# Optimization experiments

Hardware: AMD Instinct MI355X
Metric: run time of the kernel (lower is better)

## Reference

```python
import jax, jax.numpy as jnp
import numpy as np

# Axial permutations for num_dimensions=3, emb_dim=-1 (total rank 5), att_dims=[1,2,3]
PERMS = [[0, 2, 3, 1, 4], [0, 1, 3, 2, 4], [0, 1, 2, 3, 4]]
H_SELF = 8
H_CROSS = 8
E_HEAD = 64  # dims_embed[0] / (num_heads_self + num_heads_cross) = 1024/16


def layernorm(x, eps=1e-5):
    # nn.LayerNorm(elementwise_affine=False)
    m = x.mean(axis=-1, keepdims=True)
    v = x.var(axis=-1, keepdims=True)
    return (x - m) * jax.lax.rsqrt(v + eps)


def cross_attention(x, kv, wq, wkv, h, e):
    # x: [bb, t, d_q], kv: [bb, t_kv, d_kv]
    q = x @ wq                                   # [bb, t, h*e]
    k, v = jnp.split(kv @ wkv, 2, axis=-1)       # each [bb, t_kv, h*e]
    bb, t = q.shape[0], q.shape[1]
    tk = k.shape[1]
    q = q.reshape(bb, t, h, e)
    k = k.reshape(bb, tk, h, e)
    v = v.reshape(bb, tk, h, e)
    dots = jnp.einsum('bihe,bjhe->bhij', q, k) * (e ** -0.5)
    attn = jax.nn.softmax(dots, axis=-1)
    out = jnp.einsum('bhij,bjhe->bihe', attn, v)
    return out.reshape(bb, t, h * e)


def permute_to_from(x, kv, perm, wq, wkv, h, e):
    inv = list(np.argsort(perm))
    ax = jnp.transpose(x, perm)
    axkv = jnp.transpose(kv, perm)
    shape = list(ax.shape)
    shape_kv = list(axkv.shape)
    t, d = shape[-2], shape[-1]
    t_kv, d_kv = shape_kv[-2], shape_kv[-1]
    r1 = shape[1] / shape_kv[1]
    r2 = shape[2] / shape_kv[2]
    if int(r1) != 1:
        axkv = jnp.repeat(axkv, max(1, int(r1)), axis=1)
        ax = jnp.repeat(ax, max(1, int(1.0 / r1)), axis=1)
    if int(r2) != 1:
        axkv = jnp.repeat(axkv, max(1, int(r2)), axis=2)
        ax = jnp.repeat(ax, max(1, int(1.0 / r2)), axis=2)
    assert ax.shape[1:3] == axkv.shape[1:3]
    perm_shape = list(ax.shape)
    out = cross_attention(ax.reshape(-1, t, d), axkv.reshape(-1, t_kv, d_kv), wq, wkv, h, e)
    out = out.reshape(perm_shape[:-1] + [-1])
    if shape[1] < shape_kv[1]:  # field0 coarser along perm dim 1 -> mean-pool back
        out = out.reshape(shape[:2] + [int(1.0 / r1)] + perm_shape[2:-1] + [-1]).mean(axis=2)
    if shape[2] < shape_kv[2]:
        out = out.reshape(shape[:3] + [int(1.0 / r2)] + perm_shape[3:-1] + [-1]).mean(axis=3)
    out = out.reshape(shape[:-1] + [-1])
    return jnp.transpose(out, inv)


def setup_inputs() -> dict:
    key = jax.random.key(0)
    ks = jax.random.split(key, 8)
    B, T, LA, LO, D0, D1 = 32, 12, 12, 12, 1024, 512
    s = 0.02
    return {
        'x0': jax.random.normal(ks[0], (B, T, LA, LO, D0), dtype=jnp.float32),
        'x1': jax.random.normal(ks[1], (B, T, LA // 2, LO // 2, D1), dtype=jnp.float32),
        'wq_self': jax.random.normal(ks[2], (3, D0, 512), dtype=jnp.float32) * s,
        'wkv_self': jax.random.normal(ks[3], (3, D0, 1024), dtype=jnp.float32) * s,
        'wq_cross': jax.random.normal(ks[4], (3, D0, 512), dtype=jnp.float32) * s,
        'wkv_cross': jax.random.normal(ks[5], (3, D1, 1024), dtype=jnp.float32) * s,
        'w_out': jax.random.normal(ks[6], (3, 1024, D0), dtype=jnp.float32) * s,
        'b_out': jnp.zeros((3, D0), dtype=jnp.float32),
    }


def reference(x0, x1, wq_self, wkv_self, wq_cross, wkv_cross, w_out, b_out):
    pass_through = x0
    f0 = layernorm(x0)
    f1 = layernorm(x1)
    for ip, perm in enumerate(PERMS):
        o_self = permute_to_from(f0, f0, perm, wq_self[ip], wkv_self[ip], H_SELF, E_HEAD)
        o_cross = permute_to_from(f0, f1, perm, wq_cross[ip], wkv_cross[ip], H_CROSS, E_HEAD)
        f0 = jnp.concatenate([o_self, o_cross], axis=-1) @ w_out[ip] + b_out[ip]
    return pass_through + f0
```

## Files before the change

### kernel.cpp

```cpp
#include <hip/hip_runtime.h>
#include <hip/hip_bf16.h>


typedef __bf16 bf16x8 __attribute__((ext_vector_type(8)));
typedef float floatx4 __attribute__((ext_vector_type(4)));
typedef float floatx16 __attribute__((ext_vector_type(16)));

#define N0 55296
#define N1 13824

#define RAW_BARRIER() asm volatile("s_barrier" ::: "memory")
#define VMCNT(n) asm volatile("s_waitcnt vmcnt(" #n ")" ::: "memory")

__device__ __forceinline__ void gload16(const void* g, void* l) {
    __builtin_amdgcn_global_load_lds(
        (const __attribute__((address_space(1))) unsigned int*)g,
        (__attribute__((address_space(3))) unsigned int*)l, 16, 0, 0);
}

template <int SIG>
__device__ __forceinline__ int mapRow(int i) {
    if (SIG == 0) return i;
    const int b = i / 1728, r = i % 1728;
    const int d1 = r / 144, r2 = r % 144, d2 = r2 / 12, d3 = r2 % 12;
    if (SIG == 1) return b * 1728 + d3 * 144 + d1 * 12 + d2;
    if (SIG == 2) return b * 1728 + d3 * 144 + d2 * 12 + d1;
    return b * 1728 + d1 * 144 + d3 * 12 + d2;
}

template <int D>
__device__ __forceinline__ void ln_body(const float* __restrict__ xr,
                                        __hip_bfloat16* __restrict__ yr)
{
    constexpr int V = D / 256;
    const int tid = threadIdx.x;
    float vals[V];
    if constexpr (V == 4) {
        const float4 t4 = *(const float4*)(xr + tid * 4);
        vals[0] = t4.x; vals[1] = t4.y; vals[2] = t4.z; vals[3] = t4.w;
    } else {
        const float2 t2 = *(const float2*)(xr + tid * 2);
        vals[0] = t2.x; vals[1] = t2.y;
    }
    float s = 0.f, q = 0.f;
#pragma unroll
    for (int k = 0; k < V; ++k) { s += vals[k]; q += vals[k] * vals[k]; }
#pragma unroll
    for (int off = 32; off > 0; off >>= 1) {
        s += __shfl_xor(s, off);
        q += __shfl_xor(q, off);
    }
    __shared__ float rs[4], rq[4];
    const int w = tid >> 6;
    if ((tid & 63) == 0) { rs[w] = s; rq[w] = q; }
    __syncthreads();
    s = rs[0] + rs[1] + rs[2] + rs[3];
    q = rq[0] + rq[1] + rq[2] + rq[3];
    const float mean = s * (1.f / D);
    const float var  = q * (1.f / D) - mean * mean;
    const float rstd = rsqrtf(var + 1e-5f);
    __hip_bfloat16 o[V];
#pragma unroll
    for (int k = 0; k < V; ++k) o[k] = __float2bfloat16((vals[k] - mean) * rstd);
    if constexpr (V == 4) *(uint2*)(yr + tid * 4) = *(const uint2*)o;
    else                  *(uint*)(yr + tid * 2)  = *(const uint*)o;
}

__global__ __launch_bounds__(256)
void ln_all(const float* __restrict__ x0, const float* __restrict__ x1,
            __hip_bfloat16* __restrict__ f0, __hip_bfloat16* __restrict__ f1)
{
    const int row = blockIdx.x;
    if (row < N0) {
        ln_body<1024>(x0 + (size_t)row * 1024, f0 + (size_t)row * 1024);
    } else {
        const int r = row - N0;
        ln_body<512>(x1 + (size_t)r * 512, f1 + (size_t)r * 512);
    }
}

__global__ __launch_bounds__(256)
void transpose_all(const float* __restrict__ wqs, const float* __restrict__ wkvs,
                   const float* __restrict__ wqc, const float* __restrict__ wkvc,
                   const float* __restrict__ wo,
                   __hip_bfloat16* __restrict__ W1t,
                   __hip_bfloat16* __restrict__ W2t,
                   __hip_bfloat16* __restrict__ W3t)
{
    int idx = blockIdx.x;
    const float* src;
    __hip_bfloat16* dst;
    int K, N;
    if (idx < 1536) {
        const int ip = idx / 512; idx %= 512; K = 1024; N = 512;
        src = wqs + (size_t)ip * 524288;  dst = W1t + (size_t)ip * 2097152;
    } else if (idx < 4608) {
        idx -= 1536;
        const int ip = idx / 1024; idx %= 1024; K = 1024; N = 1024;
        src = wkvs + (size_t)ip * 1048576; dst = W1t + (size_t)ip * 2097152 + 524288;
    } else if (idx < 6144) {
        idx -= 4608;
        const int ip = idx / 512; idx %= 512; K = 1024; N = 512;
        src = wqc + (size_t)ip * 524288;  dst = W1t + (size_t)ip * 2097152 + 1572864;
    } else if (idx < 7680) {
        idx -= 6144;
        const int ip = idx / 512; idx %= 512; K = 512; N = 1024;
        src = wkvc + (size_t)ip * 524288; dst = W2t + (size_t)ip * 524288;
    } else {
        idx -= 7680;
        const int ip = idx / 1024; idx %= 1024; K = 1024; N = 1024;
        src = wo + (size_t)ip * 1048576;  dst = W3t + (size_t)ip * 1048576;
    }
    const int tiles_x = N >> 5;
    const int n0 = (idx % tiles_x) * 32, k0 = (idx / tiles_x) * 32;

    __shared__ float tile[32][33];
    const int tx = threadIdx.x & 31, ty = threadIdx.x >> 5;
#pragma unroll
    for (int d = 0; d < 4; ++d)
        tile[ty + d * 8][tx] = src[(size_t)(k0 + ty + d * 8) * N + n0 + tx];
    __syncthreads();
#pragma unroll
    for (int d = 0; d < 4; ++d)
        dst[(size_t)(n0 + ty + d * 8) * K + k0 + tx] = __float2bfloat16(tile[tx][ty + d * 8]);
}

__global__ __launch_bounds__(256)
void cast_w3o(const float* __restrict__ wo, __hip_bfloat16* __restrict__ W3o)
{
    const size_t i = ((size_t)blockIdx.x * 256 + threadIdx.x) * 4;
    const float4 v = *(const float4*)(wo + i);
    __hip_bfloat16 o[4] = { __float2bfloat16(v.x), __float2bfloat16(v.y),
                            __float2bfloat16(v.z), __float2bfloat16(v.w) };
    *(uint2*)(W3o + i) = *(const uint2*)o;
}

__global__ __launch_bounds__(256)
void bfold_kernel(const float* __restrict__ b_out,
                  const __hip_bfloat16* __restrict__ W1t,
                  float* __restrict__ bf)
{
    const int idx = blockIdx.x * 256 + threadIdx.x;
    const int j = idx >> 11, n = idx & 2047;
    const float* b = b_out + j * 1024;
    const __hip_bfloat16* w = W1t + ((size_t)(j + 1) * 2048 + n) * 1024;
    float s = 0.f;
#pragma unroll 4
    for (int d = 0; d < 1024; ++d) s += b[d] * __bfloat162float(w[d]);
    bf[idx] = s;
}

template <int EPI, int SIG>
__global__ __launch_bounds__(512)
void gemm8p(const __hip_bfloat16* __restrict__ A,
            const __hip_bfloat16* __restrict__ Bt,
            void* __restrict__ Cv,
            const float* __restrict__ bias,
            const float* __restrict__ resid,
            int M, int N, int K, int lda)
{
    __shared__ __align__(16) char lds[131072];

    const int gx  = gridDim.x;
    const int nwg = gx * gridDim.y;
    const int bid = blockIdx.y * gx + blockIdx.x;
    const int swz = (bid & 7) * (nwg >> 3) + (bid >> 3);
    const int m0 = (swz / gx) * 256;
    const int n0 = (swz % gx) * 256;

    const int t    = threadIdx.x;
    const int w    = t >> 6;
    const int lane = t & 63;
    const int wr   = w >> 2;
    const int wc   = w & 3;
    const int l31  = lane & 31;
    const int kh   = lane >> 5;

    floatx16 acc[4][2] = {};

    const int tr   = t >> 3;
    const int scol = ((t & 7) ^ (tr & 7)) << 3;
    const __hip_bfloat16* aP[4];
#pragma unroll
    for (int r = 0; r < 4; ++r)
        aP[r] = A + (size_t)mapRow<SIG>(m0 + tr + r * 64) * lda + scol;
    const __hip_bfloat16* bG = Bt + (size_t)(n0 + ((tr >> 5) * 64) + (tr & 31)) * K + scol;
    const int ldst = t * 16;

    const int sw   = ((kh ^ (l31 & 7)) << 4);
    const int aOfs = wr * 8192 + l31 * 128 + sw;
    const int bOfs = 32768 + (wc * 32 + l31) * 128 + sw;

    auto stageA = [&](char* buf, int h, int ka) {
        gload16(aP[h]     + ka, buf + h * 16384 + ldst);
        gload16(aP[h + 2] + ka, buf + h * 16384 + 8192 + ldst);
    };
    auto stageB = [&](char* buf, int h, int kb) {
        gload16(bG + kb + (size_t)(h * 32)       * K, buf + 32768 + h * 16384 + ldst);
        gload16(bG + kb + (size_t)(h * 32 + 128) * K, buf + 32768 + h * 16384 + 8192 + ldst);
    };

    const char* bufC = lds;
    auto ldA = [&](int h, bf16x8 (&a)[2][4]) {
#pragma unroll
        for (int mf = 0; mf < 2; ++mf)
#pragma unroll
            for (int ks = 0; ks < 4; ++ks)
                a[mf][ks] = *(const bf16x8*)(bufC + ((h * 16384 + mf * 4096 + aOfs) ^ (ks * 32)));
    };
    auto ldB = [&](int h, bf16x8 (&b)[4]) {
#pragma unroll
        for (int ks = 0; ks < 4; ++ks)
            b[ks] = *(const bf16x8*)(bufC + ((h * 16384 + bOfs) ^ (ks * 32)));
    };
    auto quad = [&](bf16x8 (&a)[2][4], bf16x8 (&b)[4], int mbase, int nf) {
        __builtin_amdgcn_s_setprio(1);
#pragma unroll
        for (int ks = 0; ks < 4; ++ks)
#pragma unroll
            for (int mf = 0; mf < 2; ++mf)
                acc[mbase + mf][nf] = __builtin_amdgcn_mfma_f32_32x32x16_bf16(
                    a[mf][ks], b[ks], acc[mbase + mf][nf], 0, 0, 0);
        __builtin_amdgcn_s_setprio(0);
    };

    const int NT = K >> 6;

    stageA(lds, 0, 0);
    stageB(lds, 0, 0);
    stageA(lds, 1, 0);
    stageB(lds, 1, 0);
    VMCNT(4);
    RAW_BARRIER();

    bf16x8 a0[2][4], a1[2][4], b0[4], b1[4];

    for (int tt = 0; tt < NT - 1; ++tt) {
        bufC = lds + ((tt & 1) << 16);
        char* bufN = lds + (((tt + 1) & 1) << 16);
        const int kc = (tt + 1) << 6;
        ldA(0, a0); ldB(0, b0);
        stageA(bufN, 0, kc);
        RAW_BARRIER(); __builtin_amdgcn_sched_barrier(0);
        quad(a0, b0, 0, 0);
        VMCNT(4); RAW_BARRIER();
        ldA(1, a1);
        stageB(bufN, 0, kc);
        RAW_BARRIER(); __builtin_amdgcn_sched_barrier(0);
        quad(a1, b0, 2, 0);
        VMCNT(4); RAW_BARRIER();
        ldB(1, b1);
        stageA(bufN, 1, kc);
        RAW_BARRIER(); __builtin_amdgcn_sched_barrier(0);
        quad(a0, b1, 0, 1);
        RAW_BARRIER();
        stageB(bufN, 1, kc);
        RAW_BARRIER(); __builtin_amdgcn_sched_barrier(0);
        quad(a1, b1, 2, 1);
        VMCNT(4); RAW_BARRIER();
    }

    bufC = lds + (((NT - 1) & 1) << 16);
    ldA(0, a0); ldB(0, b0);
    RAW_BARRIER(); __builtin_amdgcn_sched_barrier(0);
    quad(a0, b0, 0, 0);
    VMCNT(2); RAW_BARRIER();
    ldA(1, a1);
    RAW_BARRIER(); __builtin_amdgcn_sched_barrier(0);
    quad(a1, b0, 2, 0);
    VMCNT(0); RAW_BARRIER();
    ldB(1, b1);
    RAW_BARRIER(); __builtin_amdgcn_sched_barrier(0);
    quad(a0, b1, 0, 1);
    quad(a1, b1, 2, 1);

#pragma unroll
    for (int mf = 0; mf < 4; ++mf) {
#pragma unroll
        for (int nf = 0; nf < 2; ++nf) {
            const int col = n0 + wc * 64 + nf * 32 + l31;
#pragma unroll
            for (int reg = 0; reg < 16; ++reg) {
                const int row = m0 + wr * 128 + mf * 32 + (reg & 3) + ((reg >> 2) << 3) + (kh << 2);
                const size_t idx = (size_t)row * N + col;
                const float v = acc[mf][nf][reg];
                if (EPI == 0) {
                    ((__hip_bfloat16*)Cv)[idx] = __float2bfloat16(v);
                } else if (EPI == 1) {
                    ((__hip_bfloat16*)Cv)[idx] = __float2bfloat16(v + bias[col]);
                } else {
                    ((float*)Cv)[idx] = resid[idx] + v + bias[col];
                }
            }
        }
    }
}

__global__ __launch_bounds__(512)
void attn_fused(const __hip_bfloat16* __restrict__ qkv,
                const __hip_bfloat16* __restrict__ kvc,
                __hip_bfloat16* __restrict__ out, int ip)
{
    __shared__ __align__(16) __hip_bfloat16 R[12][2052];
    __shared__ __align__(16) __hip_bfloat16 KV[12][1032];
    __shared__ __hip_bfloat16 P[16][12][12];

    const int g   = blockIdx.x;
    const int tid = threadIdx.x;

    const int b  = g / 144;
    const int u1 = (g / 12) % 12;
    const int u2 = g % 12;
    int kvb, kvstride, tkc;
    if (ip == 0) {
        kvb = b * 432 + (u1 >> 1) * 6 + (u2 >> 1); kvstride = 36; tkc = 12;
    } else if (ip == 1) {
        kvb = b * 432 + u1 * 36 + (u2 >> 1); kvstride = 6; tkc = 6;
    } else {
        kvb = b * 432 + u1 * 36 + (u2 >> 1) * 6; kvstride = 1; tkc = 6;
    }

    const uint4* src = (const uint4*)(qkv + (size_t)g * 12 * 2048);
    for (int idx = tid; idx < 12 * 256; idx += 512) {
        const int row = idx >> 8, cg = idx & 255;
        *(uint4*)(&R[row][cg * 8]) = src[row * 256 + cg];
    }
    for (int idx = tid; idx < tkc * 128; idx += 512) {
        const int row = idx >> 7, cg = idx & 127;
        const uint4* kvr = (const uint4*)(kvc + (size_t)(kvb + row * kvstride) * 3072);
        *(uint4*)(&KV[row][cg * 8]) = kvr[cg];
    }
    __syncthreads();

    const int nd_self = 8 * 12 * 12;
    const int nd = nd_self + 8 * 12 * tkc;
    for (int idx = tid; idx < nd; idx += 512) {
        int h, i, j;
        const __hip_bfloat162 *q2, *k2;
        bool self = idx < nd_self;
        if (self) {
            h = idx / 144; const int rem = idx % 144; i = rem / 12; j = rem % 12;
            q2 = (const __hip_bfloat162*)(&R[i][h * 64]);
            k2 = (const __hip_bfloat162*)(&R[j][512 + h * 64]);
        } else {
            const int x = idx - nd_self;
            h = x / (12 * tkc); const int rem = x % (12 * tkc); i = rem / tkc; j = rem % tkc;
            q2 = (const __hip_bfloat162*)(&R[i][1536 + h * 64]);
            k2 = (const __hip_bfloat162*)(&KV[j][h * 64]);
        }
        float s = 0.f;
#pragma unroll
        for (int e = 0; e < 32; ++e) {
            const float2 qf = __bfloat1622float2(q2[e]);
            const float2 kf = __bfloat1622float2(k2[e]);
            s += qf.x * kf.x + qf.y * kf.y;
        }
        P[self ? h : 8 + h][i][j] = __float2bfloat16(s * 0.125f);
    }
    __syncthreads();

    if (tid < 192) {
        const int half = tid / 96, h = (tid % 96) / 12, i = tid % 12;
        const int tk = half ? tkc : 12;
        __hip_bfloat16* p = &P[half * 8 + h][i][0];
        float v[12];
        float mx = -1e30f;
        for (int j = 0; j < tk; ++j) { v[j] = __bfloat162float(p[j]); mx = fmaxf(mx, v[j]); }
        float sum = 0.f;
        for (int j = 0; j < tk; ++j) { v[j] = __expf(v[j] - mx); sum += v[j]; }
        const float inv = 1.f / sum;
        for (int j = 0; j < tk; ++j) p[j] = __float2bfloat16(v[j] * inv);
    }
    __syncthreads();

    for (int idx = tid; idx < 12 * 512; idx += 512) {
        const int i = idx >> 9, c2 = idx & 511;
        const int col = c2 * 2;
        float a0 = 0.f, a1 = 0.f;
        if (c2 < 256) {
            const int h = col >> 6;
            for (int j = 0; j < 12; ++j) {
                const float p = __bfloat162float(P[h][i][j]);
                a0 += p * __bfloat162float(R[j][1024 + col]);
                a1 += p * __bfloat162float(R[j][1024 + col + 1]);
            }
        } else {
            const int cc = col - 512;
            const int h = cc >> 6;
            for (int j = 0; j < tkc; ++j) {
                const float p = __bfloat162float(P[8 + h][i][j]);
                a0 += p * __bfloat162float(KV[j][512 + cc]);
                a1 += p * __bfloat162float(KV[j][512 + cc + 1]);
            }
        }
        __hip_bfloat16 o[2] = { __float2bfloat16(a0), __float2bfloat16(a1) };
        *(uint*)(out + (size_t)(g * 12 + i) * 1024 + col) = *(const uint*)o;
    }
}

extern "C" void kernel_launch(void* const* d_in, const int* in_sizes, int n_in,
                              void* d_out, int out_size, void* d_ws, size_t ws_size,
                              hipStream_t stream)
{
    (void)in_sizes; (void)n_in; (void)out_size; (void)ws_size;
    const float* x0        = (const float*)d_in[0];
    const float* x1        = (const float*)d_in[1];
    const float* wq_self   = (const float*)d_in[2];
    const float* wkv_self  = (const float*)d_in[3];
    const float* wq_cross  = (const float*)d_in[4];
    const float* wkv_cross = (const float*)d_in[5];
    const float* w_out     = (const float*)d_in[6];
    const float* b_out     = (const float*)d_in[7];

    __hip_bfloat16* qkv = (__hip_bfloat16*)d_out;

    char* ws = (char*)d_ws;
    size_t off = 0;
    auto alloc = [&](size_t bytes) {
        void* p = ws + off;
        off += (bytes + 255) & ~(size_t)255;
        return p;
    };
    __hip_bfloat16* f0   = (__hip_bfloat16*)alloc((size_t)N0 * 1024 * 2);
    __hip_bfloat16* f1   = (__hip_bfloat16*)alloc((size_t)N1 * 512 * 2);
    __hip_bfloat16* kvc3 = (__hip_bfloat16*)alloc((size_t)N1 * 3072 * 2);
    __hip_bfloat16* W1t  = (__hip_bfloat16*)alloc((size_t)3 * 2048 * 1024 * 2);
    __hip_bfloat16* W2t  = (__hip_bfloat16*)alloc((size_t)3 * 1024 * 512 * 2);
    __hip_bfloat16* W3t  = (__hip_bfloat16*)alloc((size_t)3 * 1024 * 1024 * 2);
    __hip_bfloat16* W3o  = (__hip_bfloat16*)alloc((size_t)2 * 1024 * 1024 * 2);
    __hip_bfloat16* Wf   = (__hip_bfloat16*)alloc((size_t)2 * 2048 * 1024 * 2);
    float*          bfo  = (float*)alloc((size_t)2 * 2048 * 4);

    ln_all<<<N0 + N1, 256, 0, stream>>>(x0, x1, f0, f1);
    transpose_all<<<10752, 256, 0, stream>>>(wq_self, wkv_self, wq_cross,
                                             wkv_cross, w_out, W1t, W2t, W3t);
    cast_w3o<<<2048, 256, 0, stream>>>(w_out, W3o);
    bfold_kernel<<<16, 256, 0, stream>>>(b_out, W1t, bfo);
    for (int j = 0; j < 2; ++j)
        gemm8p<0, 0><<<dim3(4, 8), 512, 0, stream>>>(
            W1t + (size_t)(j + 1) * 2048 * 1024, W3o + (size_t)j * 1024 * 1024,
            Wf + (size_t)j * 2048 * 1024, nullptr, nullptr, 2048, 1024, 1024, 1024);
    gemm8p<0, 0><<<dim3(12, 54), 512, 0, stream>>>(
        f1, W2t, kvc3, nullptr, nullptr, N1, 3072, 512, 512);

    gemm8p<0, 1><<<dim3(8, 216), 512, 0, stream>>>(
        f0, W1t, qkv, nullptr, nullptr, N0, 2048, 1024, 1024);
    attn_fused<<<4608, 512, 0, stream>>>(qkv, kvc3, f0, 0);

    gemm8p<1, 2><<<dim3(8, 216), 512, 0, stream>>>(
        f0, Wf, qkv, bfo, nullptr, N0, 2048, 1024, 1024);
    attn_fused<<<4608, 512, 0, stream>>>(qkv, kvc3 + 1024, f0, 1);

    gemm8p<1, 3><<<dim3(8, 216), 512, 0, stream>>>(
        f0, Wf + (size_t)2048 * 1024, qkv, bfo + 2048, nullptr, N0, 2048, 1024, 1024);
    attn_fused<<<4608, 512, 0, stream>>>(qkv, kvc3 + 2048, f0, 2);

    gemm8p<2, 0><<<dim3(4, 216), 512, 0, stream>>>(
        f0, W3t + (size_t)2 * 1024 * 1024, d_out, b_out + 2 * 1024, x0,
        N0, 1024, 1024, 1024);
}
```

Before: 1.675 ms.

## Prefetch next A fragment across iterations, rework LDS swizzle, merge weight-cast kernel

The GEMM main loop now loads the first A fragment of the next K-tile during the last quarter of the current tile and drops several redundant s_barriers, keeping only compiler sched fences. This is meant to hide LDS read latency and cut synchronisation stalls. The LDS XOR swizzle now keys on row groups of four, with a matching change to the global-to-LDS column mapping, to alter bank-conflict behaviour. The separate cast_w3o launch is folded into transpose_all as extra blocks, and that kernel now transposes only the last w_out slice, so one launch is saved. Removing barriers and reading the next buffer early both risk race conditions if the vmcnt and barrier ordering is off.

```diff
diff --git a/kernel.cpp b/kernel.cpp
--- a/kernel.cpp
+++ b/kernel.cpp
@@ -11,6 +11,7 @@
 
 #define RAW_BARRIER() asm volatile("s_barrier" ::: "memory")
 #define VMCNT(n) asm volatile("s_waitcnt vmcnt(" #n ")" ::: "memory")
+#define SCHED_FENCE() __builtin_amdgcn_sched_barrier(0)
 
 __device__ __forceinline__ void gload16(const void* g, void* l) {
     __builtin_amdgcn_global_load_lds(
@@ -85,9 +86,18 @@
                    const float* __restrict__ wo,
                    __hip_bfloat16* __restrict__ W1t,
                    __hip_bfloat16* __restrict__ W2t,
-                   __hip_bfloat16* __restrict__ W3t)
+                   __hip_bfloat16* __restrict__ W3t,
+                   __hip_bfloat16* __restrict__ W3o)
 {
     int idx = blockIdx.x;
+    if (idx >= 8704) {
+        const size_t i = ((size_t)(idx - 8704) * 256 + threadIdx.x) * 4;
+        const float4 v = *(const float4*)(wo + i);
+        __hip_bfloat16 o[4] = { __float2bfloat16(v.x), __float2bfloat16(v.y),
+                                __float2bfloat16(v.z), __float2bfloat16(v.w) };
+        *(uint2*)(W3o + i) = *(const uint2*)o;
+        return;
+    }
     const float* src;
     __hip_bfloat16* dst;
     int K, N;
@@ -108,8 +118,8 @@
         src = wkvc + (size_t)ip * 524288; dst = W2t + (size_t)ip * 524288;
     } else {
         idx -= 7680;
-        const int ip = idx / 1024; idx %= 1024; K = 1024; N = 1024;
-        src = wo + (size_t)ip * 1048576;  dst = W3t + (size_t)ip * 1048576;
+        K = 1024; N = 1024;
+        src = wo + (size_t)2 * 1048576;  dst = W3t + (size_t)2 * 1048576;
     }
     const int tiles_x = N >> 5;
     const int n0 = (idx % tiles_x) * 32, k0 = (idx / tiles_x) * 32;
@@ -123,16 +133,6 @@
 #pragma unroll
     for (int d = 0; d < 4; ++d)
         dst[(size_t)(n0 + ty + d * 8) * K + k0 + tx] = __float2bfloat16(tile[tx][ty + d * 8]);
-}
-
-__global__ __launch_bounds__(256)
-void cast_w3o(const float* __restrict__ wo, __hip_bfloat16* __restrict__ W3o)
-{
-    const size_t i = ((size_t)blockIdx.x * 256 + threadIdx.x) * 4;
-    const float4 v = *(const float4*)(wo + i);
-    __hip_bfloat16 o[4] = { __float2bfloat16(v.x), __float2bfloat16(v.y),
-                            __float2bfloat16(v.z), __float2bfloat16(v.w) };
-    *(uint2*)(W3o + i) = *(const uint2*)o;
 }
 
 __global__ __launch_bounds__(256)
@@ -179,7 +179,7 @@
     floatx16 acc[4][2] = {};
 
     const int tr   = t >> 3;
-    const int scol = ((t & 7) ^ (tr & 7)) << 3;
+    const int scol = ((t & 7) ^ ((tr >> 2) & 7)) << 3;
     const __hip_bfloat16* aP[4];
 #pragma unroll
     for (int r = 0; r < 4; ++r)
@@ -187,17 +187,19 @@
     const __hip_bfloat16* bG = Bt + (size_t)(n0 + ((tr >> 5) * 64) + (tr & 31)) * K + scol;
     const int ldst = t * 16;
 
-    const int sw   = ((kh ^ (l31 & 7)) << 4);
-    const int aOfs = wr * 8192 + l31 * 128 + sw;
-    const int bOfs = 32768 + (wc * 32 + l31) * 128 + sw;
+    const int key = (l31 >> 2) & 7;
+    const int kq  = (key >> 1) & 3;
+    const int kb  = ((kh ^ key) & 1) << 4;
+    const int aBase = wr * 8192 + l31 * 128 + kb;
+    const int bBase = 32768 + (wc * 32 + l31) * 128 + kb;
 
     auto stageA = [&](char* buf, int h, int ka) {
         gload16(aP[h]     + ka, buf + h * 16384 + ldst);
         gload16(aP[h + 2] + ka, buf + h * 16384 + 8192 + ldst);
     };
-    auto stageB = [&](char* buf, int h, int kb) {
-        gload16(bG + kb + (size_t)(h * 32)       * K, buf + 32768 + h * 16384 + ldst);
-        gload16(bG + kb + (size_t)(h * 32 + 128) * K, buf + 32768 + h * 16384 + 8192 + ldst);
+    auto stageB = [&](char* buf, int h, int kb_) {
+        gload16(bG + kb_ + (size_t)(h * 32)       * K, buf + 32768 + h * 16384 + ldst);
+        gload16(bG + kb_ + (size_t)(h * 32 + 128) * K, buf + 32768 + h * 16384 + 8192 + ldst);
     };
 
     const char* bufC = lds;
@@ -206,12 +208,12 @@
         for (int mf = 0; mf < 2; ++mf)
 #pragma unroll
             for (int ks = 0; ks < 4; ++ks)
-                a[mf][ks] = *(const bf16x8*)(bufC + ((h * 16384 + mf * 4096 + aOfs) ^ (ks * 32)));
+                a[mf][ks] = *(const bf16x8*)(bufC + h * 16384 + mf * 4096 + aBase + ((ks ^ kq) << 5));
     };
     auto ldB = [&](int h, bf16x8 (&b)[4]) {
 #pragma unroll
         for (int ks = 0; ks < 4; ++ks)
-            b[ks] = *(const bf16x8*)(bufC + ((h * 16384 + bOfs) ^ (ks * 32)));
+            b[ks] = *(const bf16x8*)(bufC + h * 16384 + bBase + ((ks ^ kq) << 5));
     };
     auto quad = [&](bf16x8 (&a)[2][4], bf16x8 (&b)[4], int mbase, int nf) {
         __builtin_amdgcn_s_setprio(1);
@@ -234,43 +236,46 @@
     RAW_BARRIER();
 
     bf16x8 a0[2][4], a1[2][4], b0[4], b1[4];
+    ldA(0, a0);
 
     for (int tt = 0; tt < NT - 1; ++tt) {
         bufC = lds + ((tt & 1) << 16);
         char* bufN = lds + (((tt + 1) & 1) << 16);
         const int kc = (tt + 1) << 6;
-        ldA(0, a0); ldB(0, b0);
+        ldB(0, b0);
         stageA(bufN, 0, kc);
-        RAW_BARRIER(); __builtin_amdgcn_sched_barrier(0);
+        SCHED_FENCE();
         quad(a0, b0, 0, 0);
         VMCNT(4); RAW_BARRIER();
         ldA(1, a1);
         stageB(bufN, 0, kc);
-        RAW_BARRIER(); __builtin_amdgcn_sched_barrier(0);
+        SCHED_FENCE();
         quad(a1, b0, 2, 0);
         VMCNT(4); RAW_BARRIER();
         ldB(1, b1);
         stageA(bufN, 1, kc);
-        RAW_BARRIER(); __builtin_amdgcn_sched_barrier(0);
+        SCHED_FENCE();
         quad(a0, b1, 0, 1);
-        RAW_BARRIER();
+        VMCNT(4); RAW_BARRIER();
+        bufC = bufN;
+        ldA(0, a0);
         stageB(bufN, 1, kc);
-        RAW_BARRIER(); __builtin_amdgcn_sched_barrier(0);
+        SCHED_FENCE();
         quad(a1, b1, 2, 1);
         VMCNT(4); RAW_BARRIER();
     }
 
     bufC = lds + (((NT - 1) & 1) << 16);
-    ldA(0, a0); ldB(0, b0);
-    RAW_BARRIER(); __builtin_amdgcn_sched_barrier(0);
+    ldB(0, b0);
+    SCHED_FENCE();
     quad(a0, b0, 0, 0);
     VMCNT(2); RAW_BARRIER();
     ldA(1, a1);
-    RAW_BARRIER(); __builtin_amdgcn_sched_barrier(0);
+    SCHED_FENCE();
     quad(a1, b0, 2, 0);
     VMCNT(0); RAW_BARRIER();
     ldB(1, b1);
-    RAW_BARRIER(); __builtin_amdgcn_sched_barrier(0);
+    SCHED_FENCE();
     quad(a0, b1, 0, 1);
     quad(a1, b1, 2, 1);
 
@@ -433,8 +438,7 @@
 
     ln_all<<<N0 + N1, 256, 0, stream>>>(x0, x1, f0, f1);
     transpose_all<<<10752, 256, 0, stream>>>(wq_self, wkv_self, wq_cross,
-                                             wkv_cross, w_out, W1t, W2t, W3t);
-    cast_w3o<<<2048, 256, 0, stream>>>(w_out, W3o);
+                                             wkv_cross, w_out, W1t, W2t, W3t, W3o);
     bfold_kernel<<<16, 256, 0, stream>>>(b_out, W1t, bfo);
     for (int j = 0; j < 2; ++j)
         gemm8p<0, 0><<<dim3(4, 8), 512, 0, stream>>>(
```

Result: faster. 1.618 ms (-3.4%).
